# Kernel tuning notes

Hardware: AMD Instinct MI355X
Metric: run time of the kernel (lower is better)

The kernel has to match this reference:

```python
import jax, jax.numpy as jnp
import numpy as np

B, LAT, H, D, T = 2048, 32, 256, 20, 512  # batch, latent, hidden, output, max_len


def setup_inputs() -> dict:
    key = jax.random.key(0)
    ks = jax.random.split(key, 16)
    s = 0.05  # weight scale
    n = lambda k, shape, sc=s: jax.random.normal(k, shape, dtype=jnp.float32) * sc
    return {
        "z": n(ks[0], (B, LAT), 1.0),
        "target_lengths": jax.random.randint(ks[1], (B,), 1, T + 1),
        "max_len": T,
        # latent -> initial hidden / cell (hidden_dim * num_layers outputs)
        "w_lh": n(ks[2], (2 * H, LAT)), "b_lh": n(ks[3], (2 * H,)),
        "w_lc": n(ks[4], (2 * H, LAT)), "b_lc": n(ks[5], (2 * H,)),
        # LSTM layer 0 (input = output_dim), gates ordered i,f,g,o (PyTorch)
        "w_ih0": n(ks[6], (4 * H, D)), "w_hh0": n(ks[7], (4 * H, H)),
        "b_ih0": n(ks[8], (4 * H,)), "b_hh0": n(ks[9], (4 * H,)),
        # LSTM layer 1 (input = hidden_dim)
        "w_ih1": n(ks[10], (4 * H, H)), "w_hh1": n(ks[11], (4 * H, H)),
        "b_ih1": n(ks[12], (4 * H,)), "b_hh1": n(ks[13], (4 * H,)),
        # output projection
        "w_proj": n(ks[14], (D, H)), "b_proj": n(ks[15], (D,)),
    }


def _lstm_cell(x, h, c, w_ih, w_hh, b_ih, b_hh):
    g = x @ w_ih.T + b_ih + h @ w_hh.T + b_hh  # [B, 4H]
    i, f, gg, o = jnp.split(g, 4, axis=-1)
    c = jax.nn.sigmoid(f) * c + jax.nn.sigmoid(i) * jnp.tanh(gg)
    h = jax.nn.sigmoid(o) * jnp.tanh(c)
    return h, c


def reference(z, target_lengths, max_len,
              w_lh, b_lh, w_lc, b_lc,
              w_ih0, w_hh0, b_ih0, b_hh0,
              w_ih1, w_hh1, b_ih1, b_hh1,
              w_proj, b_proj):
    batch = z.shape[0]
    hid = w_hh0.shape[1]
    out_dim = w_ih0.shape[1]
    # initial per-layer states: view(B, num_layers, H)
    h_init = (z @ w_lh.T + b_lh).reshape(batch, 2, hid)
    c_init = (z @ w_lc.T + b_lc).reshape(batch, 2, hid)
    h0, h1 = h_init[:, 0], h_init[:, 1]
    c0, c1 = c_init[:, 0], c_init[:, 1]
    x0 = jnp.zeros((batch, out_dim), dtype=z.dtype)

    def step(carry, _):
        x, h0, c0, h1, c1 = carry
        h0, c0 = _lstm_cell(x, h0, c0, w_ih0, w_hh0, b_ih0, b_hh0)
        h1, c1 = _lstm_cell(h0, h1, c1, w_ih1, w_hh1, b_ih1, b_hh1)
        y = h1 @ w_proj.T + b_proj  # [B, D], fed back as next input
        return (y, h0, c0, h1, c1), y

    _, ys = jax.lax.scan(step, (x0, h0, c0, h1, c1), None, length=int(max_len))
    return jnp.transpose(ys, (1, 0, 2))  # [B, T, D]
```

## Files before the change

kernel.cpp:

```cpp
#include <hip/hip_runtime.h>
#include <hip/hip_bf16.h>

#define NB 32
#define TT 512
#define DD 20

using bf16x8 = __attribute__((ext_vector_type(8))) short;
using f32x4  = __attribute__((ext_vector_type(4))) float;

typedef __attribute__((address_space(3))) unsigned int lds_uint;
typedef __attribute__((address_space(1))) unsigned int glob_uint;

#define OFF_WSTR  0
#define OFF_WPROJ 1638400
#define OFF_B0    1654784
#define OFF_B1    1658880
#define OFF_EXCH  1662976
#define OFF_FLAG  3760128
#define WS_NEED_QUAD 3762176
#define WQUARTER  409600
#define WSTR_BYTES 1638400

#define QM_H0    0
#define QM_H1    16896
#define QM_XB    33792
#define QM_WPS   35840
#define QM_ZB    52224
#define QM_RING  56320
#define QM_TOTAL 121856

#define SM_RING  0
#define SM_H0    98304
#define SM_H1    115200
#define SM_XB    132096
#define SM_WPS   134144
#define SM_ZB    150528
#define SM_TOTAL 154624

__device__ __forceinline__ float sigf(float x) { return 1.0f / (1.0f + __expf(-x)); }
__device__ __forceinline__ float tanhfast(float x) { return 1.0f - 2.0f / (__expf(2.0f * x) + 1.0f); }

__device__ __forceinline__ void stage16(const char* g, const char* l) {
    __builtin_amdgcn_global_load_lds((glob_uint*)g, (lds_uint*)l, 16, 0, 0);
}

#define BARRIER_LK do { \
    asm volatile("s_waitcnt lgkmcnt(0)" ::: "memory"); \
    __builtin_amdgcn_s_barrier(); \
    asm volatile("" ::: "memory"); \
    __builtin_amdgcn_sched_barrier(0); \
} while (0)

__global__ void prep_quad(const float* __restrict__ wih0, const float* __restrict__ whh0,
                          const float* __restrict__ wih1, const float* __restrict__ whh1,
                          const float* __restrict__ wproj,
                          const float* __restrict__ bih0, const float* __restrict__ bhh0,
                          const float* __restrict__ bih1, const float* __restrict__ bhh1,
                          char* __restrict__ ws) {
    int idx = blockIdx.x * 256 + threadIdx.x;
    if (idx < 819200) {
        int g  = idx / 204800;
        int r  = idx - g * 204800;
        int u  = r >> 13;
        int r2 = r & 8191;
        int w  = r2 >> 11;
        int r3 = r2 & 2047;
        int q  = r3 >> 9;
        int e2 = r3 & 511;
        const float* src; int K, kt;
        if (u < 8)       { src = whh0; K = 256; kt = u; }
        else if (u == 8) { src = wih0; K = 20;  kt = 0; }
        else if (u < 17) { src = whh1; K = 256; kt = u - 9; }
        else             { src = wih1; K = 256; kt = u - 17; }
        int NT = q * 16 + g * 4 + w;
        int j = e2 & 7, lane = e2 >> 3;
        int n = NT * 16 + (lane & 15);
        int k = kt * 32 + ((lane >> 4) << 3) + j;
        float v = (k < K) ? src[n * K + k] : 0.0f;
        ((__hip_bfloat16*)(ws + OFF_WSTR))[idx] = __float2bfloat16(v);
    } else if (idx < 827392) {
        int e = idx - 819200;
        int j = e & 7, lane = (e >> 3) & 63, tile = e >> 9;
        int kt = tile & 7, nt = tile >> 3;
        int n = nt * 16 + (lane & 15);
        int k = kt * 32 + ((lane >> 4) << 3) + j;
        float v = (n < 20) ? wproj[n * 256 + k] : 0.0f;
        ((__hip_bfloat16*)(ws + OFF_WPROJ))[e] = __float2bfloat16(v);
    } else if (idx < 828416) {
        int j = idx - 827392; ((float*)(ws + OFF_B0))[j] = bih0[j] + bhh0[j];
    } else if (idx < 829440) {
        int j = idx - 828416; ((float*)(ws + OFF_B1))[j] = bih1[j] + bhh1[j];
    } else if (idx < 829952) {
        ((unsigned int*)(ws + OFF_FLAG))[idx - 829440] = 0;
    }
}

__global__ __launch_bounds__(256, 1) void decoder_quad(
    const float* __restrict__ z, const float* __restrict__ w_lh, const float* __restrict__ b_lh,
    const float* __restrict__ w_lc, const float* __restrict__ b_lc,
    const float* __restrict__ b_proj, char* __restrict__ ws,
    float* __restrict__ out) {

    __shared__ __align__(16) char smem[QM_TOTAL];

    const int tid = threadIdx.x;
    const int grp = blockIdx.x & 63;
    const int g   = blockIdx.x >> 6;
    const int b0  = grp * NB;

    __hip_bfloat16* h0p = (__hip_bfloat16*)(smem + QM_H0);
    __hip_bfloat16* h1p = (__hip_bfloat16*)(smem + QM_H1);
    __hip_bfloat16* xbh = (__hip_bfloat16*)(smem + QM_XB);

    {
        float* zbf = (float*)(smem + QM_ZB);
        #pragma unroll
        for (int i = 0; i < 4; i++) {
            int ii = tid + i * 256;
            zbf[ii] = z[(b0 + (ii >> 5)) * 32 + (ii & 31)];
        }
        ((unsigned int*)(smem + QM_XB))[tid]       = 0;
        ((unsigned int*)(smem + QM_XB))[tid + 256] = 0;
        const bf16x8* sp = (const bf16x8*)(ws + OFF_WPROJ);
        bf16x8* dp = (bf16x8*)(smem + QM_WPS);
        #pragma unroll
        for (int i = 0; i < 4; i++) dp[tid + i * 256] = sp[tid + i * 256];
    }
    __syncthreads();

    {
        float* cinitf = (float*)(smem + QM_RING);
        const float* zbf = (const float*)(smem + QM_ZB);
        for (int ii = 0; ii < 64; ii++) {
            int pi = ii * 256 + tid;
            int b = pi >> 9, col = pi & 511;
            float dh = b_lh[col], dc = b_lc[col];
            #pragma unroll 8
            for (int k = 0; k < 32; k++) {
                float zv = zbf[b * 32 + k];
                dh += zv * w_lh[col * 32 + k];
                dc += zv * w_lc[col * 32 + k];
            }
            if (col < 256) { h0p[b * 264 + col]         = __float2bfloat16(dh); cinitf[b * 256 + col]                 = dc; }
            else           { h1p[b * 264 + (col - 256)] = __float2bfloat16(dh); cinitf[8192 + b * 256 + (col - 256)] = dc; }
        }
    }
    __syncthreads();

    const int w  = tid >> 6, ln = tid & 63;
    const int l15 = ln & 15, lq = ln >> 4;
    const int lnoff = ln * 16;
    const int colg = g * 64 + w * 16 + l15;

    float c0r[2][4], c1r[2][4];
    {
        const float* cinitf = (const float*)(smem + QM_RING);
        #pragma unroll
        for (int mt = 0; mt < 2; mt++)
            #pragma unroll
            for (int r = 0; r < 4; r++) {
                int m = mt * 16 + lq * 4 + r;
                c0r[mt][r] = cinitf[m * 256 + colg];
                c1r[mt][r] = cinitf[8192 + m * 256 + colg];
            }
    }
    __syncthreads();

    const float* bias0 = (const float*)(ws + OFF_B0);
    const float* bias1 = (const float*)(ws + OFF_B1);
    float bs0[4], bs1[4];
    #pragma unroll
    for (int q = 0; q < 4; q++) {
        bs0[q] = bias0[q * 256 + colg];
        bs1[q] = bias1[q * 256 + colg];
    }
    const int pc_nt = w & 1, pc_mt = w >> 1;
    const int pc_col = pc_nt * 16 + l15;
    const float bpj = (pc_col < 20) ? b_proj[pc_col] : 0.0f;

    const char* wps_c = smem + QM_WPS;
    const char* h0c = smem + QM_H0;
    const char* h1c = smem + QM_H1;
    const char* xbc = smem + QM_XB;
    float* outp = out;

    const char* wgl   = ws + OFF_WSTR + g * WQUARTER + w * 4096 + lnoff;
    char*       ringb = smem + QM_RING + w * 12288;
    const char* ringc = smem + QM_RING + w * 12288 + lnoff;
    int sOff = 2 * 16384;
    int slS  = 2;
    int slR  = 0;

    f32x4 acc[4][2];

    auto doKt = [&](const char* hsrc, int kt, bool isX) {
        bf16x8 af0, af1;
        if (isX) {
            af0 = *(const bf16x8*)(xbc + l15 * 64 + lq * 16);
            af1 = *(const bf16x8*)(xbc + (16 + l15) * 64 + lq * 16);
        } else {
            af0 = *(const bf16x8*)(hsrc + l15 * 528 + kt * 64 + lq * 16);
            af1 = *(const bf16x8*)(hsrc + (16 + l15) * 528 + kt * 64 + lq * 16);
        }
        #pragma unroll
        for (int q = 0; q < 4; q++)
            stage16(wgl + sOff + q * 1024, ringb + slS * 4096 + q * 1024);
        sOff += 16384; if (sOff >= WQUARTER) sOff = 0;
        slS = (slS == 2) ? 0 : slS + 1;
        asm volatile("s_waitcnt vmcnt(8)" ::: "memory");
        const char* rb = ringc + slR * 4096;
        slR = (slR == 2) ? 0 : slR + 1;
        bf16x8 w0 = *(const bf16x8*)(rb);
        bf16x8 w1 = *(const bf16x8*)(rb + 1024);
        bf16x8 w2 = *(const bf16x8*)(rb + 2048);
        bf16x8 w3 = *(const bf16x8*)(rb + 3072);
        acc[0][0] = __builtin_amdgcn_mfma_f32_16x16x32_bf16(af0, w0, acc[0][0], 0, 0, 0);
        acc[0][1] = __builtin_amdgcn_mfma_f32_16x16x32_bf16(af1, w0, acc[0][1], 0, 0, 0);
        acc[1][0] = __builtin_amdgcn_mfma_f32_16x16x32_bf16(af0, w1, acc[1][0], 0, 0, 0);
        acc[1][1] = __builtin_amdgcn_mfma_f32_16x16x32_bf16(af1, w1, acc[1][1], 0, 0, 0);
        acc[2][0] = __builtin_amdgcn_mfma_f32_16x16x32_bf16(af0, w2, acc[2][0], 0, 0, 0);
        acc[2][1] = __builtin_amdgcn_mfma_f32_16x16x32_bf16(af1, w2, acc[2][1], 0, 0, 0);
        acc[3][0] = __builtin_amdgcn_mfma_f32_16x16x32_bf16(af0, w3, acc[3][0], 0, 0, 0);
        acc[3][1] = __builtin_amdgcn_mfma_f32_16x16x32_bf16(af1, w3, acc[3][1], 0, 0, 0);
    };

    auto phaseC = [&](int t) {
        f32x4 py = {bpj, bpj, bpj, bpj};
        #pragma unroll
        for (int kt = 0; kt < 8; kt++) {
            bf16x8 ah = *(const bf16x8*)(h1c + (pc_mt * 16 + l15) * 528 + kt * 64 + lq * 16);
            bf16x8 wf = *(const bf16x8*)(wps_c + pc_nt * 8192 + kt * 1024 + lnoff);
            py = __builtin_amdgcn_mfma_f32_16x16x32_bf16(ah, wf, py, 0, 0, 0);
        }
        if (pc_col < 20) {
            #pragma unroll
            for (int r = 0; r < 4; r++) {
                int row = pc_mt * 16 + lq * 4 + r;
                if (g == 0)
                    outp[((size_t)(b0 + row) * TT + (t - 1)) * DD + pc_col] = py[r];
                xbh[row * 32 + pc_col] = __float2bfloat16(py[r]);
            }
        }
    };

    unsigned int* exBase = (unsigned int*)(ws + OFF_EXCH);
    unsigned int* flBase = (unsigned int*)(ws + OFF_FLAG);

    auto exchStore = [&](int L, const char* hp, int t) {
        unsigned int* exO = exBase + ((grp * 2 + L) * 4 + g) * 1024;
        unsigned int* flO = flBase + (grp * 2 + L) * 4 + g;
        #pragma unroll
        for (int i = 0; i < 4; i++) {
            int wi = tid * 4 + i, m = wi >> 5, cp = wi & 31;
            unsigned int v = *(const unsigned int*)(hp + m * 528 + g * 128 + cp * 4);
            __hip_atomic_store(&exO[wi], v, __ATOMIC_RELAXED, __HIP_MEMORY_SCOPE_AGENT);
        }
        asm volatile("s_waitcnt vmcnt(0)" ::: "memory");
        if (tid == 0)
            __hip_atomic_store(flO, (unsigned int)(t + 1), __ATOMIC_RELAXED, __HIP_MEMORY_SCOPE_AGENT);
    };

    auto exchFinish = [&](int L, char* hp, unsigned int expect) {
        if (tid < 3) {
            int p = tid + (tid >= g);
            unsigned int* flP = flBase + (grp * 2 + L) * 4 + p;
            int spins = 0;
            while (__hip_atomic_load(flP, __ATOMIC_RELAXED, __HIP_MEMORY_SCOPE_AGENT) < expect) {
                __builtin_amdgcn_s_sleep(8);
                if (++spins > (1 << 14)) break;
            }
        }
        BARRIER_LK;
        #pragma unroll
        for (int pp = 0; pp < 3; pp++) {
            int p = pp + (pp >= g);
            unsigned int* exP = exBase + ((grp * 2 + L) * 4 + p) * 1024;
            unsigned int pv[4];
            #pragma unroll
            for (int i = 0; i < 4; i++)
                pv[i] = __hip_atomic_load(&exP[tid * 4 + i], __ATOMIC_RELAXED, __HIP_MEMORY_SCOPE_AGENT);
            #pragma unroll
            for (int i = 0; i < 4; i++) {
                int wi = tid * 4 + i, m = wi >> 5, cp = wi & 31;
                *(unsigned int*)(hp + m * 528 + p * 128 + cp * 4) = pv[i];
            }
        }
        BARRIER_LK;
    };

    #pragma unroll
    for (int q = 0; q < 4; q++) stage16(wgl + q * 1024,         ringb + q * 1024);
    #pragma unroll
    for (int q = 0; q < 4; q++) stage16(wgl + 16384 + q * 1024, ringb + 4096 + q * 1024);

    #pragma unroll 1
    for (int t = 0; t < TT; t++) {
        #pragma unroll
        for (int q = 0; q < 4; q++) {
            f32x4 v = {bs0[q], bs0[q], bs0[q], bs0[q]};
            acc[q][0] = v; acc[q][1] = v;
        }
        #pragma unroll 1
        for (int kt = 0; kt < 7; kt++) doKt(h0c, kt, false);
        if (t > 0) {
            exchFinish(1, (char*)(smem + QM_H1), (unsigned int)t);
            phaseC(t);
        }
        doKt(h0c, 7, false);
        BARRIER_LK;
        doKt(xbc, 0, true);
        BARRIER_LK;

        #pragma unroll
        for (int mt = 0; mt < 2; mt++)
            #pragma unroll
            for (int r = 0; r < 4; r++) {
                float iv = acc[0][mt][r], fv = acc[1][mt][r];
                float gv = acc[2][mt][r], ov = acc[3][mt][r];
                float cn = sigf(fv) * c0r[mt][r] + sigf(iv) * tanhfast(gv);
                float hn = sigf(ov) * tanhfast(cn);
                c0r[mt][r] = cn;
                h0p[(mt * 16 + lq * 4 + r) * 264 + colg] = __float2bfloat16(hn);
            }
        BARRIER_LK;
        exchStore(0, h0c, t);

        #pragma unroll
        for (int q = 0; q < 4; q++) {
            f32x4 v = {bs1[q], bs1[q], bs1[q], bs1[q]};
            acc[q][0] = v; acc[q][1] = v;
        }
        #pragma unroll 1
        for (int kt = 0; kt < 8; kt++) doKt(h1c, kt, false);
        exchFinish(0, (char*)(smem + QM_H0), (unsigned int)(t + 1));
        #pragma unroll 1
        for (int kt = 0; kt < 8; kt++) doKt(h0c, kt, false);
        BARRIER_LK;

        #pragma unroll
        for (int mt = 0; mt < 2; mt++)
            #pragma unroll
            for (int r = 0; r < 4; r++) {
                float iv = acc[0][mt][r], fv = acc[1][mt][r];
                float gv = acc[2][mt][r], ov = acc[3][mt][r];
                float cn = sigf(fv) * c1r[mt][r] + sigf(iv) * tanhfast(gv);
                float hn = sigf(ov) * tanhfast(cn);
                c1r[mt][r] = cn;
                h1p[(mt * 16 + lq * 4 + r) * 264 + colg] = __float2bfloat16(hn);
            }
        BARRIER_LK;
        exchStore(1, h1c, t);
    }

    exchFinish(1, (char*)(smem + QM_H1), (unsigned int)TT);
    phaseC(TT);
}


__global__ void prep_solo(const float* __restrict__ wih0, const float* __restrict__ whh0,
                          const float* __restrict__ wih1, const float* __restrict__ whh1,
                          const float* __restrict__ wproj,
                          const float* __restrict__ bih0, const float* __restrict__ bhh0,
                          const float* __restrict__ bih1, const float* __restrict__ bhh1,
                          char* __restrict__ ws) {
    int idx = blockIdx.x * 256 + threadIdx.x;
    if (idx < 819200) {
        int s  = idx >> 12;
        int wv = (idx >> 9) & 7;
        int e2 = idx & 511;
        int u = s >> 2, qq = s & 3, half = u & 1;
        const float* src; int K, kt;
        if (u < 16)      { src = whh0; K = 256; kt = u >> 1; }
        else if (u < 18) { src = wih0; K = 20;  kt = 0; }
        else if (u < 34) { src = wih1; K = 256; kt = (u - 18) >> 1; }
        else             { src = whh1; K = 256; kt = (u - 34) >> 1; }
        int NT = half * 32 + (qq >> 1) * 16 + wv * 2 + (qq & 1);
        int j = e2 & 7, lane = e2 >> 3;
        int n = NT * 16 + (lane & 15);
        int k = kt * 32 + ((lane >> 4) << 3) + j;
        float v = (k < K) ? src[n * K + k] : 0.0f;
        ((__hip_bfloat16*)(ws + OFF_WSTR))[idx] = __float2bfloat16(v);
    } else if (idx < 827392) {
        int e = idx - 819200;
        int j = e & 7, lane = (e >> 3) & 63, tile = e >> 9;
        int kt = tile & 7, nt = tile >> 3;
        int n = nt * 16 + (lane & 15);
        int k = kt * 32 + ((lane >> 4) << 3) + j;
        float v = (n < 20) ? wproj[n * 256 + k] : 0.0f;
        ((__hip_bfloat16*)(ws + OFF_WPROJ))[e] = __float2bfloat16(v);
    } else if (idx < 828416) {
        int j = idx - 827392; ((float*)(ws + OFF_B0))[j] = bih0[j] + bhh0[j];
    } else if (idx < 829440) {
        int j = idx - 828416; ((float*)(ws + OFF_B1))[j] = bih1[j] + bhh1[j];
    }
}

__global__ __launch_bounds__(512, 1) void decoder_solo(
    const float* __restrict__ z, const float* __restrict__ w_lh, const float* __restrict__ b_lh,
    const float* __restrict__ w_lc, const float* __restrict__ b_lc,
    const float* __restrict__ b_proj, const char* __restrict__ ws,
    float* __restrict__ out) {

    __shared__ __align__(16) char smem[SM_TOTAL];

    const int tid = threadIdx.x;
    const int b0  = blockIdx.x * NB;

    __hip_bfloat16* h0p = (__hip_bfloat16*)(smem + SM_H0);
    __hip_bfloat16* h1p = (__hip_bfloat16*)(smem + SM_H1);
    __hip_bfloat16* xbh = (__hip_bfloat16*)(smem + SM_XB);

    {
        float* zbf = (float*)(smem + SM_ZB);
        zbf[tid]       = z[(b0 + (tid >> 5)) * 32 + (tid & 31)];
        int i2 = tid + 512;
        zbf[i2]        = z[(b0 + (i2 >> 5)) * 32 + (i2 & 31)];
        ((unsigned int*)(smem + SM_XB))[tid] = 0;
        const bf16x8* sp = (const bf16x8*)(ws + OFF_WPROJ);
        bf16x8* dp = (bf16x8*)(smem + SM_WPS);
        dp[tid] = sp[tid];
        dp[tid + 512] = sp[tid + 512];
    }
    __syncthreads();

    {
        float* cinitf = (float*)smem;
        const float* zbf = (const float*)(smem + SM_ZB);
        for (int ii = 0; ii < 32; ii++) {
            int pi = ii * 512 + tid;
            int b = pi >> 9, col = pi & 511;
            float dh = b_lh[col], dc = b_lc[col];
            #pragma unroll 8
            for (int k = 0; k < 32; k++) {
                float zv = zbf[b * 32 + k];
                dh += zv * w_lh[col * 32 + k];
                dc += zv * w_lc[col * 32 + k];
            }
            if (col < 256) { h0p[b * 264 + col]         = __float2bfloat16(dh); cinitf[b * 256 + col]                 = dc; }
            else           { h1p[b * 264 + (col - 256)] = __float2bfloat16(dh); cinitf[8192 + b * 256 + (col - 256)] = dc; }
        }
    }
    __syncthreads();

    const int wv = tid >> 6, ln = tid & 63;
    const int l15 = ln & 15, lq = ln >> 4;
    const int lnoff = ln * 16;

    float c0r[2][2][4], c1r[2][2][4];
    {
        const float* cinitf = (const float*)smem;
        #pragma unroll
        for (int mt = 0; mt < 2; mt++)
            #pragma unroll
            for (int h = 0; h < 2; h++)
                #pragma unroll
                for (int r = 0; r < 4; r++) {
                    int m = mt * 16 + lq * 4 + r, u = wv * 32 + h * 16 + l15;
                    c0r[mt][h][r] = cinitf[m * 256 + u];
                    c1r[mt][h][r] = cinitf[8192 + m * 256 + u];
                }
    }
    __syncthreads();

    const float* bias0 = (const float*)(ws + OFF_B0);
    const float* bias1 = (const float*)(ws + OFF_B1);
    float bs0[8], bs1[8];
    #pragma unroll
    for (int q = 0; q < 8; q++) {
        int col = (q >> 1) * 256 + wv * 32 + (q & 1) * 16 + l15;
        bs0[q] = bias0[col];
        bs1[q] = bias1[col];
    }
    const int pc_nt = wv & 1, pc_mt = wv >> 1;
    const int pc_col = pc_nt * 16 + l15;
    const float bpj = (wv < 4 && pc_col < 20) ? b_proj[pc_col] : 0.0f;

    const char* wps_c = smem + SM_WPS;
    const char* h0c = smem + SM_H0;
    const char* h1c = smem + SM_H1;
    const char* xbc = smem + SM_XB;

    float* outp = out;

    const char* wgl   = ws + OFF_WSTR + wv * 1024 + lnoff;
    char*       ringb = smem + SM_RING + wv * 12288;
    const char* ringc = smem + SM_RING + wv * 12288 + lnoff;
    int sOff = 2 * 32768;
    int slS  = 2;
    int slR  = 0;

    f32x4 acc[8][2];

    auto doPanel = [&](const char* hsrc, int kt, bool isX, int qbase) {
        bf16x8 af0, af1;
        if (isX) {
            af0 = *(const bf16x8*)(xbc + l15 * 64 + lq * 16);
            af1 = *(const bf16x8*)(xbc + (16 + l15) * 64 + lq * 16);
        } else {
            af0 = *(const bf16x8*)(hsrc + l15 * 528 + kt * 64 + lq * 16);
            af1 = *(const bf16x8*)(hsrc + (16 + l15) * 528 + kt * 64 + lq * 16);
        }
        #pragma unroll
        for (int j = 0; j < 4; j++)
            stage16(wgl + (sOff + j * 8192), ringb + slS * 4096 + j * 1024);
        sOff += 32768; if (sOff >= WSTR_BYTES) sOff = 0;
        slS = (slS == 2) ? 0 : slS + 1;
        asm volatile("s_waitcnt vmcnt(8)" ::: "memory");
        __builtin_amdgcn_sched_barrier(0);
        const char* rb = ringc + slR * 4096;
        slR = (slR == 2) ? 0 : slR + 1;
        bf16x8 w0 = *(const bf16x8*)(rb);
        bf16x8 w1 = *(const bf16x8*)(rb + 1024);
        bf16x8 w2 = *(const bf16x8*)(rb + 2048);
        bf16x8 w3 = *(const bf16x8*)(rb + 3072);
        acc[qbase + 0][0] = __builtin_amdgcn_mfma_f32_16x16x32_bf16(af0, w0, acc[qbase + 0][0], 0, 0, 0);
        acc[qbase + 0][1] = __builtin_amdgcn_mfma_f32_16x16x32_bf16(af1, w0, acc[qbase + 0][1], 0, 0, 0);
        acc[qbase + 1][0] = __builtin_amdgcn_mfma_f32_16x16x32_bf16(af0, w1, acc[qbase + 1][0], 0, 0, 0);
        acc[qbase + 1][1] = __builtin_amdgcn_mfma_f32_16x16x32_bf16(af1, w1, acc[qbase + 1][1], 0, 0, 0);
        acc[qbase + 2][0] = __builtin_amdgcn_mfma_f32_16x16x32_bf16(af0, w2, acc[qbase + 2][0], 0, 0, 0);
        acc[qbase + 2][1] = __builtin_amdgcn_mfma_f32_16x16x32_bf16(af1, w2, acc[qbase + 2][1], 0, 0, 0);
        acc[qbase + 3][0] = __builtin_amdgcn_mfma_f32_16x16x32_bf16(af0, w3, acc[qbase + 3][0], 0, 0, 0);
        acc[qbase + 3][1] = __builtin_amdgcn_mfma_f32_16x16x32_bf16(af1, w3, acc[qbase + 3][1], 0, 0, 0);
    };

    auto phaseC = [&](int t) {
        f32x4 py = {bpj, bpj, bpj, bpj};
        #pragma unroll
        for (int kt = 0; kt < 8; kt++) {
            bf16x8 ah = *(const bf16x8*)(h1c + (pc_mt * 16 + l15) * 528 + kt * 64 + lq * 16);
            bf16x8 wf = *(const bf16x8*)(wps_c + pc_nt * 8192 + kt * 1024 + lnoff);
            py = __builtin_amdgcn_mfma_f32_16x16x32_bf16(ah, wf, py, 0, 0, 0);
        }
        if (pc_col < 20) {
            #pragma unroll
            for (int r = 0; r < 4; r++) {
                int row = pc_mt * 16 + lq * 4 + r;
                outp[((size_t)(b0 + row) * TT + (t - 1)) * DD + pc_col] = py[r];
                xbh[row * 32 + pc_col] = __float2bfloat16(py[r]);
            }
        }
    };

    #pragma unroll
    for (int j = 0; j < 4; j++) stage16(wgl + j * 8192,         ringb + j * 1024);
    #pragma unroll
    for (int j = 0; j < 4; j++) stage16(wgl + 32768 + j * 8192, ringb + 4096 + j * 1024);

    #pragma unroll 1
    for (int t = 0; t < TT; t++) {
        #pragma unroll
        for (int q = 0; q < 8; q++) {
            f32x4 v = {bs0[q], bs0[q], bs0[q], bs0[q]};
            acc[q][0] = v; acc[q][1] = v;
        }
        if (t > 0 && wv < 4) phaseC(t);
        #pragma unroll 1
        for (int uu = 0; uu < 7; uu++) {
            doPanel(h0c, uu, false, 0);
            doPanel(h0c, uu, false, 4);
        }
        BARRIER_LK;
        doPanel(h0c, 7, false, 0);
        doPanel(h0c, 7, false, 4);
        doPanel(xbc, 0, true,  0);
        doPanel(xbc, 0, true,  4);
        BARRIER_LK;

        #pragma unroll
        for (int mt = 0; mt < 2; mt++)
            #pragma unroll
            for (int h = 0; h < 2; h++)
                #pragma unroll
                for (int r = 0; r < 4; r++) {
                    float iv = acc[0 + h][mt][r], fv = acc[2 + h][mt][r];
                    float gv = acc[4 + h][mt][r], ov = acc[6 + h][mt][r];
                    float cn = sigf(fv) * c0r[mt][h][r] + sigf(iv) * tanhfast(gv);
                    float hn = sigf(ov) * tanhfast(cn);
                    c0r[mt][h][r] = cn;
                    h0p[(mt * 16 + lq * 4 + r) * 264 + wv * 32 + h * 16 + l15] = __float2bfloat16(hn);
                }
        BARRIER_LK;

        #pragma unroll
        for (int q = 0; q < 8; q++) {
            f32x4 v = {bs1[q], bs1[q], bs1[q], bs1[q]};
            acc[q][0] = v; acc[q][1] = v;
        }
        #pragma unroll 1
        for (int uu = 0; uu < 8; uu++) {
            doPanel(h0c, uu, false, 0);
            doPanel(h0c, uu, false, 4);
        }
        #pragma unroll 1
        for (int uu = 0; uu < 8; uu++) {
            doPanel(h1c, uu, false, 0);
            doPanel(h1c, uu, false, 4);
        }
        BARRIER_LK;

        #pragma unroll
        for (int mt = 0; mt < 2; mt++)
            #pragma unroll
            for (int h = 0; h < 2; h++)
                #pragma unroll
                for (int r = 0; r < 4; r++) {
                    float iv = acc[0 + h][mt][r], fv = acc[2 + h][mt][r];
                    float gv = acc[4 + h][mt][r], ov = acc[6 + h][mt][r];
                    float cn = sigf(fv) * c1r[mt][h][r] + sigf(iv) * tanhfast(gv);
                    float hn = sigf(ov) * tanhfast(cn);
                    c1r[mt][h][r] = cn;
                    h1p[(mt * 16 + lq * 4 + r) * 264 + wv * 32 + h * 16 + l15] = __float2bfloat16(hn);
                }
        BARRIER_LK;
    }

    if (wv < 4) phaseC(TT);
}


extern "C" void kernel_launch(void* const* d_in, const int* in_sizes, int n_in,
                              void* d_out, int out_size, void* d_ws, size_t ws_size,
                              hipStream_t stream) {
    const float* z      = (const float*)d_in[0];
    const float* w_lh   = (const float*)d_in[3];
    const float* b_lh   = (const float*)d_in[4];
    const float* w_lc   = (const float*)d_in[5];
    const float* b_lc   = (const float*)d_in[6];
    const float* w_ih0  = (const float*)d_in[7];
    const float* w_hh0  = (const float*)d_in[8];
    const float* b_ih0  = (const float*)d_in[9];
    const float* b_hh0  = (const float*)d_in[10];
    const float* w_ih1  = (const float*)d_in[11];
    const float* w_hh1  = (const float*)d_in[12];
    const float* b_ih1  = (const float*)d_in[13];
    const float* b_hh1  = (const float*)d_in[14];
    const float* w_proj = (const float*)d_in[15];
    const float* b_proj = (const float*)d_in[16];
    char* ws = (char*)d_ws;
    float* out = (float*)d_out;

    if (ws_size >= (size_t)WS_NEED_QUAD) {
        prep_quad<<<3242, 256, 0, stream>>>(w_ih0, w_hh0, w_ih1, w_hh1, w_proj,
                                            b_ih0, b_hh0, b_ih1, b_hh1, ws);
        decoder_quad<<<256, 256, 0, stream>>>(z, w_lh, b_lh, w_lc, b_lc, b_proj, ws, out);
    } else {
        prep_solo<<<3240, 256, 0, stream>>>(w_ih0, w_hh0, w_ih1, w_hh1, w_proj,
                                            b_ih0, b_hh0, b_ih1, b_hh1, ws);
        decoder_solo<<<64, 512, 0, stream>>>(z, w_lh, b_lh, w_lc, b_lc, b_proj, ws, out);
    }
}
```

Measured before the change: 6.400 ms.

## Software-pipeline weight and activation fragment loads with a four-slot LDS ring

Replaces the per-k-tile lambda with macros that prefetch the next tile's weight and activation fragments into registers before the current tile's MFMAs are issued. The per-wave LDS weight ring grows from three to four slots, so the global-to-LDS staging runs further ahead. A sched_barrier after the vmcnt wait pins the instruction order. The aim is to hide LDS and global load latency behind MFMA work. In exchange it uses more LDS per wave and more registers, and it also lowers the spin-wait timeout, which risks breaking out of a cross-block sync wait early.

```diff
diff --git a/kernel.cpp b/kernel.cpp
--- a/kernel.cpp
+++ b/kernel.cpp
@@ -185,44 +185,57 @@
     float* outp = out;
 
     const char* wgl   = ws + OFF_WSTR + g * WQUARTER + w * 4096 + lnoff;
-    char*       ringb = smem + QM_RING + w * 12288;
-    const char* ringc = smem + QM_RING + w * 12288 + lnoff;
-    int sOff = 2 * 16384;
-    int slS  = 2;
+    char*       ringb = smem + QM_RING + w * 16384;
+    const char* ringc = smem + QM_RING + w * 16384 + lnoff;
+    int sOff = 0;
+    int slS  = 0;
     int slR  = 0;
 
     f32x4 acc[4][2];
-
-    auto doKt = [&](const char* hsrc, int kt, bool isX) {
-        bf16x8 af0, af1;
-        if (isX) {
-            af0 = *(const bf16x8*)(xbc + l15 * 64 + lq * 16);
-            af1 = *(const bf16x8*)(xbc + (16 + l15) * 64 + lq * 16);
-        } else {
-            af0 = *(const bf16x8*)(hsrc + l15 * 528 + kt * 64 + lq * 16);
-            af1 = *(const bf16x8*)(hsrc + (16 + l15) * 528 + kt * 64 + lq * 16);
-        }
-        #pragma unroll
-        for (int q = 0; q < 4; q++)
-            stage16(wgl + sOff + q * 1024, ringb + slS * 4096 + q * 1024);
-        sOff += 16384; if (sOff >= WQUARTER) sOff = 0;
-        slS = (slS == 2) ? 0 : slS + 1;
-        asm volatile("s_waitcnt vmcnt(8)" ::: "memory");
-        const char* rb = ringc + slR * 4096;
-        slR = (slR == 2) ? 0 : slR + 1;
-        bf16x8 w0 = *(const bf16x8*)(rb);
-        bf16x8 w1 = *(const bf16x8*)(rb + 1024);
-        bf16x8 w2 = *(const bf16x8*)(rb + 2048);
-        bf16x8 w3 = *(const bf16x8*)(rb + 3072);
-        acc[0][0] = __builtin_amdgcn_mfma_f32_16x16x32_bf16(af0, w0, acc[0][0], 0, 0, 0);
-        acc[0][1] = __builtin_amdgcn_mfma_f32_16x16x32_bf16(af1, w0, acc[0][1], 0, 0, 0);
-        acc[1][0] = __builtin_amdgcn_mfma_f32_16x16x32_bf16(af0, w1, acc[1][0], 0, 0, 0);
-        acc[1][1] = __builtin_amdgcn_mfma_f32_16x16x32_bf16(af1, w1, acc[1][1], 0, 0, 0);
-        acc[2][0] = __builtin_amdgcn_mfma_f32_16x16x32_bf16(af0, w2, acc[2][0], 0, 0, 0);
-        acc[2][1] = __builtin_amdgcn_mfma_f32_16x16x32_bf16(af1, w2, acc[2][1], 0, 0, 0);
-        acc[3][0] = __builtin_amdgcn_mfma_f32_16x16x32_bf16(af0, w3, acc[3][0], 0, 0, 0);
-        acc[3][1] = __builtin_amdgcn_mfma_f32_16x16x32_bf16(af1, w3, acc[3][1], 0, 0, 0);
-    };
+    bf16x8 wT0, wT1, wT2, wT3, afA, afB;
+
+#define STAGE_NEXT do { \
+    stage16(wgl + sOff,        ringb + slS * 4096); \
+    stage16(wgl + sOff + 1024, ringb + slS * 4096 + 1024); \
+    stage16(wgl + sOff + 2048, ringb + slS * 4096 + 2048); \
+    stage16(wgl + sOff + 3072, ringb + slS * 4096 + 3072); \
+    sOff += 16384; if (sOff >= WQUARTER) sOff = 0; \
+    slS = (slS + 1) & 3; \
+} while (0)
+
+#define WWAIT do { \
+    asm volatile("s_waitcnt vmcnt(8)" ::: "memory"); \
+    __builtin_amdgcn_sched_barrier(0); \
+} while (0)
+
+#define LOADW do { \
+    const char* rb_ = ringc + slR * 4096; slR = (slR + 1) & 3; \
+    wT0 = *(const bf16x8*)(rb_); \
+    wT1 = *(const bf16x8*)(rb_ + 1024); \
+    wT2 = *(const bf16x8*)(rb_ + 2048); \
+    wT3 = *(const bf16x8*)(rb_ + 3072); \
+} while (0)
+
+#define LOADA(hsrc, ktv) do { \
+    afA = *(const bf16x8*)((hsrc) + l15 * 528 + (ktv) * 64 + lq * 16); \
+    afB = *(const bf16x8*)((hsrc) + (16 + l15) * 528 + (ktv) * 64 + lq * 16); \
+} while (0)
+
+#define LOADAX do { \
+    afA = *(const bf16x8*)(xbc + l15 * 64 + lq * 16); \
+    afB = *(const bf16x8*)(xbc + (16 + l15) * 64 + lq * 16); \
+} while (0)
+
+#define MFMA8 do { \
+    acc[0][0] = __builtin_amdgcn_mfma_f32_16x16x32_bf16(afA, wT0, acc[0][0], 0, 0, 0); \
+    acc[0][1] = __builtin_amdgcn_mfma_f32_16x16x32_bf16(afB, wT0, acc[0][1], 0, 0, 0); \
+    acc[1][0] = __builtin_amdgcn_mfma_f32_16x16x32_bf16(afA, wT1, acc[1][0], 0, 0, 0); \
+    acc[1][1] = __builtin_amdgcn_mfma_f32_16x16x32_bf16(afB, wT1, acc[1][1], 0, 0, 0); \
+    acc[2][0] = __builtin_amdgcn_mfma_f32_16x16x32_bf16(afA, wT2, acc[2][0], 0, 0, 0); \
+    acc[2][1] = __builtin_amdgcn_mfma_f32_16x16x32_bf16(afB, wT2, acc[2][1], 0, 0, 0); \
+    acc[3][0] = __builtin_amdgcn_mfma_f32_16x16x32_bf16(afA, wT3, acc[3][0], 0, 0, 0); \
+    acc[3][1] = __builtin_amdgcn_mfma_f32_16x16x32_bf16(afB, wT3, acc[3][1], 0, 0, 0); \
+} while (0)
 
     auto phaseC = [&](int t) {
         f32x4 py = {bpj, bpj, bpj, bpj};
@@ -267,7 +280,7 @@
             int spins = 0;
             while (__hip_atomic_load(flP, __ATOMIC_RELAXED, __HIP_MEMORY_SCOPE_AGENT) < expect) {
                 __builtin_amdgcn_s_sleep(8);
-                if (++spins > (1 << 14)) break;
+                if (++spins > (1 << 11)) break;
             }
         }
         BARRIER_LK;
@@ -288,10 +301,12 @@
         BARRIER_LK;
     };
 
-    #pragma unroll
-    for (int q = 0; q < 4; q++) stage16(wgl + q * 1024,         ringb + q * 1024);
-    #pragma unroll
-    for (int q = 0; q < 4; q++) stage16(wgl + 16384 + q * 1024, ringb + 4096 + q * 1024);
+    STAGE_NEXT;
+    STAGE_NEXT;
+    STAGE_NEXT;
+    WWAIT;
+    LOADW;
+    LOADA(h0c, 0);
 
     #pragma unroll 1
     for (int t = 0; t < TT; t++) {
@@ -301,14 +316,16 @@
             acc[q][0] = v; acc[q][1] = v;
         }
         #pragma unroll 1
-        for (int kt = 0; kt < 7; kt++) doKt(h0c, kt, false);
+        for (int kt = 0; kt < 7; kt++) {
+            STAGE_NEXT; MFMA8; WWAIT; LOADW; LOADA(h0c, kt + 1);
+        }
         if (t > 0) {
             exchFinish(1, (char*)(smem + QM_H1), (unsigned int)t);
             phaseC(t);
         }
-        doKt(h0c, 7, false);
-        BARRIER_LK;
-        doKt(xbc, 0, true);
+        BARRIER_LK;
+        STAGE_NEXT; MFMA8; WWAIT; LOADW; LOADAX;
+        STAGE_NEXT; MFMA8; WWAIT; LOADW; LOADA(h1c, 0);
         BARRIER_LK;
 
         #pragma unroll
@@ -331,10 +348,17 @@
             acc[q][0] = v; acc[q][1] = v;
         }
         #pragma unroll 1
-        for (int kt = 0; kt < 8; kt++) doKt(h1c, kt, false);
+        for (int kt = 0; kt < 7; kt++) {
+            STAGE_NEXT; MFMA8; WWAIT; LOADW; LOADA(h1c, kt + 1);
+        }
+        STAGE_NEXT; MFMA8; WWAIT; LOADW;
         exchFinish(0, (char*)(smem + QM_H0), (unsigned int)(t + 1));
+        LOADA(h0c, 0);
         #pragma unroll 1
-        for (int kt = 0; kt < 8; kt++) doKt(h0c, kt, false);
+        for (int kt = 0; kt < 7; kt++) {
+            STAGE_NEXT; MFMA8; WWAIT; LOADW; LOADA(h0c, kt + 1);
+        }
+        STAGE_NEXT; MFMA8; WWAIT; LOADW; LOADA(h0c, 0);
         BARRIER_LK;
 
         #pragma unroll
@@ -354,6 +378,13 @@
 
     exchFinish(1, (char*)(smem + QM_H1), (unsigned int)TT);
     phaseC(TT);
+
+#undef STAGE_NEXT
+#undef WWAIT
+#undef LOADW
+#undef LOADA
+#undef LOADAX
+#undef MFMA8
 }
 
 
```

New measurement: 6.163 ms. -3.7%, faster.
